# Performance work log

Hardware: AMD Instinct MI355X
Metric: run time of the kernel (lower is better)

Reference implementation:

```python
import jax, jax.numpy as jnp
import numpy as np
from functools import partial

B = 256          # batch_size (== hidden_dim, required by the module's broadcasting)
T = 512          # seq_length
H = 256          # hidden_dim == dim_out
E = 6            # emb_dim
V = 10           # num_input_digits
C = 10           # num_classes


def _kaiming(key, shape):
    fan_in = shape[1]
    return jax.random.normal(key, shape, dtype=jnp.float32) * np.sqrt(2.0 / fan_in)


def setup_inputs() -> dict:
    key = jax.random.key(0)
    ks = jax.random.split(key, 12)
    inp = {
        "x": jax.random.randint(ks[0], (B, T), 0, V),
        "emb": jax.random.normal(ks[1], (V, E), dtype=jnp.float32),
        "Wxg": _kaiming(ks[2], (H, E)), "Whg": _kaiming(ks[3], (H, H)), "bg": jnp.zeros((H,), jnp.float32),
        "Wxi": _kaiming(ks[4], (H, E)), "Whi": _kaiming(ks[5], (H, H)), "bi": jnp.zeros((H,), jnp.float32),
        "Wxf": _kaiming(ks[6], (H, E)), "Whf": _kaiming(ks[7], (H, H)), "bf": jnp.zeros((H,), jnp.float32),
        "Wxo": _kaiming(ks[8], (H, E)), "Who": _kaiming(ks[9], (H, H)), "bo": jnp.zeros((H,), jnp.float32),
        "Wp": _kaiming(ks[10], (C, H)), "bp": jnp.zeros((C,), jnp.float32),
    }
    return inp


def reference(x, emb, Wxg, Whg, bg, Wxi, Whi, bi, Wxf, Whf, bf, Wxo, Who, bo, Wp, bp):
    # x: (B, T) int -> embed -> (B, T, E)
    xe = emb[x]
    # time-major (T, E, B): each step uses x_t.T as in the torch code
    xt_seq = jnp.transpose(xe, (1, 2, 0))

    h0 = jnp.zeros((H, B), jnp.float32)  # h lives as (H, B) per original math
    c0 = jnp.zeros((H, B), jnp.float32)

    def step(carry, xTt):  # xTt: (E, B)
        h, c = carry
        # NOTE: bias (H,) broadcasts over the trailing batch axis (H==B), faithful
        # to the original torch broadcasting.
        g = jnp.tanh(Wxg @ xTt + Whg @ h + bg)
        i = jax.nn.sigmoid(Wxi @ xTt + Whi @ h + bi)
        f = jax.nn.sigmoid(Wxf @ xTt + Whf @ h + bf)
        o = jax.nn.sigmoid(Wxo @ xTt + Who @ h + bo)
        c = g * i + c * f
        h = jnp.tanh(c) * o
        return (h, c), None

    (h, c), _ = jax.lax.scan(step, (h0, c0), xt_seq)
    return (Wp @ h).T + bp  # (B, C)
```

## Files before the change

### kernel.cpp

```cpp
#include <hip/hip_runtime.h>
#include <hip/hip_bf16.h>


typedef __attribute__((ext_vector_type(4))) int   int4v;
typedef __attribute__((ext_vector_type(4))) float float4v;

#define MFMA_I8(a, b, c) __builtin_amdgcn_mfma_i32_16x16x64_i8(a, b, c, 0, 0, 0)

#define K_TANH (-2.8853900817779268f)
#define K_SIG  (-1.4426950408889634f)

__device__ __forceinline__ short f2b(float f) {
    __hip_bfloat16 b = __float2bfloat16(f); return *(short*)&b;
}
__device__ __forceinline__ float b2f(short s) {
    union { unsigned int u; float f; } v; v.u = ((unsigned int)(unsigned short)s) << 16; return v.f;
}
__device__ __forceinline__ float fexp2(float x) {
#if __has_builtin(__builtin_amdgcn_exp2f)
    return __builtin_amdgcn_exp2f(x);
#else
    return __expf(x * 0.6931471805599453f);
#endif
}
__device__ __forceinline__ float frcp(float x) { return __builtin_amdgcn_rcpf(x); }

__global__ __attribute__((amdgpu_flat_work_group_size(512, 512), amdgpu_waves_per_eu(2, 2)))
void lstm_i8(
    const int* __restrict__ x,
    const float* __restrict__ emb,
    const float* __restrict__ Wxg, const float* __restrict__ Whg, const float* __restrict__ bg,
    const float* __restrict__ Wxi, const float* __restrict__ Whi, const float* __restrict__ bi,
    const float* __restrict__ Wxf, const float* __restrict__ Whf, const float* __restrict__ bff,
    const float* __restrict__ Wxo, const float* __restrict__ Who, const float* __restrict__ bo,
    const float* __restrict__ Wp, const float* __restrict__ bp,
    float* __restrict__ out)
{
    const int tid = threadIdx.x, bid = blockIdx.x;
    const int c0 = bid * 2;
    const int w = tid >> 6, lane = tid & 63;
    const int l = lane & 15, q = lane >> 4;
    const int col = l & 1;
    const int g3  = (l >> 1) & 7;
    const int si  = g3 & 3;
    const int srr = g3 >> 2;
    const int rw  = 32 * w;
    const int row = rw + 16 * srr + 4 * q + si;

    __shared__ __align__(16) unsigned int hbuf[2][2 * 272 / 4];
    __shared__ __align__(16) short hfin[2 * 264];
    __shared__ unsigned char xdig2[512 * 2];
    __shared__ __align__(16) float tblf[256 * 44];
    __shared__ float scaleL[4 * 256];

    const float* WxT[4] = {Wxg, Wxi, Wxf, Wxo};
    const float* WhT[4] = {Whg, Whi, Whf, Who};

    if (tid < 2 * 272 / 4) hbuf[0][tid] = 0u;
    for (int i = tid; i < 1024; i += 512)
        xdig2[i] = (unsigned char)x[(c0 + (i & 1)) * 512 + (i >> 1)];

    for (int i = tid; i < 2560; i += 512) {
        int r = i / 10, d = i - r * 10;
        float4v v;
        #pragma unroll
        for (int g = 0; g < 4; g++) {
            float s = 0.f;
            #pragma unroll
            for (int e = 0; e < 6; e++) s += WxT[g][r * 6 + e] * emb[d * 6 + e];
            v[g] = s * (g == 0 ? K_TANH : K_SIG);
        }
        *(float4v*)&tblf[r * 44 + d * 4] = v;
    }

    int4v wa[4][2][4];
    #pragma unroll
    for (int g = 0; g < 4; g++)
        #pragma unroll
        for (int rr = 0; rr < 2; rr++) {
            const float* Wr = WhT[g] + (rw + 16 * rr + l) * 256 + q * 16;
            float mx = 0.f;
            #pragma unroll
            for (int kt = 0; kt < 4; kt++)
                #pragma unroll
                for (int c4 = 0; c4 < 4; c4++) {
                    float4v v = *(const float4v*)(Wr + kt * 64 + c4 * 4);
                    #pragma unroll
                    for (int j = 0; j < 4; j++) mx = fmaxf(mx, fabsf(v[j]));
                }
            mx = fmaxf(mx, __shfl_xor(mx, 16));
            mx = fmaxf(mx, __shfl_xor(mx, 32));
            mx = fmaxf(mx, 1e-20f);
            if (q == 0) scaleL[g * 256 + rw + 16 * rr + l] = mx;
            float qs = 127.f / mx;
            #pragma unroll
            for (int kt = 0; kt < 4; kt++) {
                int4v f;
                #pragma unroll
                for (int dw = 0; dw < 4; dw++) {
                    float4v v = *(const float4v*)(Wr + kt * 64 + dw * 4);
                    int word = 0;
                    #pragma unroll
                    for (int byt = 0; byt < 4; byt++) {
                        int z = (int)rintf(v[byt] * qs);
                        word |= (z & 255) << (8 * byt);
                    }
                    f[dw] = word;
                }
                wa[g][rr][kt] = f;
            }
        }

    __syncthreads();

    float dscl[4];
    #pragma unroll
    for (int g = 0; g < 4; g++) {
        float kk = (g == 0 ? K_TANH : K_SIG) * (1.f / 16129.f);
        dscl[g] = scaleL[g * 256 + row] * kk;
    }
    float bSc[4];
    bSc[0] = bg[c0 + col] * K_TANH; bSc[1] = bi[c0 + col] * K_SIG;
    bSc[2] = bff[c0 + col] * K_SIG; bSc[3] = bo[c0 + col] * K_SIG;

    const bool bi1 = (si & 1) != 0;
    const bool bi2 = (si & 2) != 0;
    const bool brr = (srr != 0);
    const float* tprow = &tblf[row * 44];

    float cs = 0.f, hl = 0.f;

    for (int t = 0; t < 512; t++) {
        const int p = t & 1;
        const char* hbase = (const char*)hbuf[p] + col * 272 + q * 16;

        int4v acc[4][2];
        #pragma unroll
        for (int g = 0; g < 4; g++)
            #pragma unroll
            for (int rr = 0; rr < 2; rr++)
                acc[g][rr] = (int4v){0, 0, 0, 0};

        int dg = xdig2[t * 2 + col];
        float4v tb = *(const float4v*)(tprow + dg * 4);

        #pragma unroll
        for (int kt = 0; kt < 4; kt++) {
            int4v hf = *(const int4v*)(hbase + kt * 64);
            #pragma unroll
            for (int g = 0; g < 4; g++) {
                acc[g][0] = MFMA_I8(wa[g][0][kt], hf, acc[g][0]);
                acc[g][1] = MFMA_I8(wa[g][1][kt], hf, acc[g][1]);
            }
        }

        int av[4];
        #pragma unroll
        for (int g = 0; g < 4; g++) {
            int s00 = bi1 ? acc[g][0][1] : acc[g][0][0];
            int s01 = bi1 ? acc[g][0][3] : acc[g][0][2];
            int s10 = bi1 ? acc[g][1][1] : acc[g][1][0];
            int s11 = bi1 ? acc[g][1][3] : acc[g][1][2];
            int s0  = bi2 ? s01 : s00;
            int s1  = bi2 ? s11 : s10;
            av[g]   = brr ? s1 : s0;
        }
        {
            float pg = fmaf((float)av[0], dscl[0], tb[0] + bSc[0]);
            float pi = fmaf((float)av[1], dscl[1], tb[1] + bSc[1]);
            float pf = fmaf((float)av[2], dscl[2], tb[2] + bSc[2]);
            float po = fmaf((float)av[3], dscl[3], tb[3] + bSc[3]);
            float gg = fmaf(2.f, frcp(1.f + fexp2(pg)), -1.f);
            float ii = frcp(1.f + fexp2(pi));
            float ff = frcp(1.f + fexp2(pf));
            float oo = frcp(1.f + fexp2(po));
            float c  = fmaf(gg, ii, cs * ff);
            cs = c;
            float th = fmaf(2.f, frcp(1.f + fexp2(K_TANH * c)), -1.f);
            float hh = th * oo;
            hl = hh;
            int hq = (int)rintf(hh * 127.f);
            *((char*)hbuf[1 - p] + col * 272 + row) = (char)hq;
        }
        __syncthreads();
    }

    hfin[col * 264 + row] = f2b(hl);
    __syncthreads();

    if (tid < 20) {
        int pc = tid / 10, cls = tid - pc * 10;
        const short* hcol = &hfin[pc * 264];
        const float* wrow = Wp + cls * 256;
        float s = 0.f;
        #pragma unroll 8
        for (int k = 0; k < 256; k++) s += b2f(hcol[k]) * wrow[k];
        out[(c0 + pc) * 10 + cls] = s + bp[cls];
    }
}

extern "C" void kernel_launch(void* const* d_in, const int* in_sizes, int n_in,
                              void* d_out, int out_size, void* d_ws, size_t ws_size,
                              hipStream_t stream) {
    const int*   x   = (const int*)d_in[0];
    const float* emb = (const float*)d_in[1];
    const float* Wxg = (const float*)d_in[2];
    const float* Whg = (const float*)d_in[3];
    const float* bg  = (const float*)d_in[4];
    const float* Wxi = (const float*)d_in[5];
    const float* Whi = (const float*)d_in[6];
    const float* bi  = (const float*)d_in[7];
    const float* Wxf = (const float*)d_in[8];
    const float* Whf = (const float*)d_in[9];
    const float* bff = (const float*)d_in[10];
    const float* Wxo = (const float*)d_in[11];
    const float* Who = (const float*)d_in[12];
    const float* bo  = (const float*)d_in[13];
    const float* Wp  = (const float*)d_in[14];
    const float* bp  = (const float*)d_in[15];

    hipLaunchKernelGGL(lstm_i8, dim3(128), dim3(512), 0, stream,
                       x, emb, Wxg, Whg, bg, Wxi, Whi, bi, Wxf, Whf, bff,
                       Wxo, Who, bo, Wp, bp, (float*)d_out);
}
```

Baseline: 611.0 us.

## Pack h bytes via shuffles, transpose input table, merge reciprocals in gates

Each step now writes the quantized hidden state as one packed 32-bit word per four rows, built from lane shuffles, instead of four separate byte stores. The hbuf stride is changed and the per-digit input table becomes digit-major. The gate math merges reciprocals: tanh(g)*sigmoid(i) and tanh(c)*sigmoid(o) each take a single rcp of a product, with pre-activations clamped so the products cannot overflow. The aim is fewer LDS stores and bank conflicts and fewer transcendental ops on the serial per-step path, at the cost of extra shuffle latency.

```diff
diff --git a/kernel.cpp b/kernel.cpp
--- a/kernel.cpp
+++ b/kernel.cpp
@@ -9,6 +9,8 @@
 
 #define K_TANH (-2.8853900817779268f)
 #define K_SIG  (-1.4426950408889634f)
+
+#define HSTRIDE 320
 
 __device__ __forceinline__ short f2b(float f) {
     __hip_bfloat16 b = __float2bfloat16(f); return *(short*)&b;
@@ -24,6 +26,7 @@
 #endif
 }
 __device__ __forceinline__ float frcp(float x) { return __builtin_amdgcn_rcpf(x); }
+__device__ __forceinline__ float clamp60(float x) { return __builtin_amdgcn_fmed3f(x, -60.f, 60.f); }
 
 __global__ __attribute__((amdgpu_flat_work_group_size(512, 512), amdgpu_waves_per_eu(2, 2)))
 void lstm_i8(
@@ -47,21 +50,21 @@
     const int rw  = 32 * w;
     const int row = rw + 16 * srr + 4 * q + si;
 
-    __shared__ __align__(16) unsigned int hbuf[2][2 * 272 / 4];
+    __shared__ __align__(16) unsigned int hbuf[2][2 * HSTRIDE / 4];
     __shared__ __align__(16) short hfin[2 * 264];
     __shared__ unsigned char xdig2[512 * 2];
-    __shared__ __align__(16) float tblf[256 * 44];
+    __shared__ __align__(16) float tblT[10 * 1024];
     __shared__ float scaleL[4 * 256];
 
     const float* WxT[4] = {Wxg, Wxi, Wxf, Wxo};
     const float* WhT[4] = {Whg, Whi, Whf, Who};
 
-    if (tid < 2 * 272 / 4) hbuf[0][tid] = 0u;
+    if (tid < 2 * HSTRIDE / 4) hbuf[0][tid] = 0u;
     for (int i = tid; i < 1024; i += 512)
         xdig2[i] = (unsigned char)x[(c0 + (i & 1)) * 512 + (i >> 1)];
 
     for (int i = tid; i < 2560; i += 512) {
-        int r = i / 10, d = i - r * 10;
+        int d = i >> 8, r = i & 255;
         float4v v;
         #pragma unroll
         for (int g = 0; g < 4; g++) {
@@ -70,7 +73,7 @@
             for (int e = 0; e < 6; e++) s += WxT[g][r * 6 + e] * emb[d * 6 + e];
             v[g] = s * (g == 0 ? K_TANH : K_SIG);
         }
-        *(float4v*)&tblf[r * 44 + d * 4] = v;
+        *(float4v*)&tblT[d * 1024 + r * 4] = v;
     }
 
     int4v wa[4][2][4];
@@ -126,13 +129,14 @@
     const bool bi1 = (si & 1) != 0;
     const bool bi2 = (si & 2) != 0;
     const bool brr = (srr != 0);
-    const float* tprow = &tblf[row * 44];
+    const float* tprow = tblT + row * 4;
+    const int hoff = col * HSTRIDE + rw + 16 * srr + 4 * q;
 
     float cs = 0.f, hl = 0.f;
 
     for (int t = 0; t < 512; t++) {
         const int p = t & 1;
-        const char* hbase = (const char*)hbuf[p] + col * 272 + q * 16;
+        const char* hbase = (const char*)hbuf[p] + col * HSTRIDE + q * 16;
 
         int4v acc[4][2];
         #pragma unroll
@@ -142,7 +146,7 @@
                 acc[g][rr] = (int4v){0, 0, 0, 0};
 
         int dg = xdig2[t * 2 + col];
-        float4v tb = *(const float4v*)(tprow + dg * 4);
+        float4v tb = *(const float4v*)(tprow + dg * 1024);
 
         #pragma unroll
         for (int kt = 0; kt < 4; kt++) {
@@ -166,21 +170,22 @@
             av[g]   = brr ? s1 : s0;
         }
         {
-            float pg = fmaf((float)av[0], dscl[0], tb[0] + bSc[0]);
-            float pi = fmaf((float)av[1], dscl[1], tb[1] + bSc[1]);
-            float pf = fmaf((float)av[2], dscl[2], tb[2] + bSc[2]);
-            float po = fmaf((float)av[3], dscl[3], tb[3] + bSc[3]);
-            float gg = fmaf(2.f, frcp(1.f + fexp2(pg)), -1.f);
-            float ii = frcp(1.f + fexp2(pi));
-            float ff = frcp(1.f + fexp2(pf));
-            float oo = frcp(1.f + fexp2(po));
-            float c  = fmaf(gg, ii, cs * ff);
+            float pg = clamp60(fmaf((float)av[0], dscl[0], tb[0] + bSc[0]));
+            float pi = clamp60(fmaf((float)av[1], dscl[1], tb[1] + bSc[1]));
+            float pf = clamp60(fmaf((float)av[2], dscl[2], tb[2] + bSc[2]));
+            float po = clamp60(fmaf((float)av[3], dscl[3], tb[3] + bSc[3]));
+            float Eg = fexp2(pg), Ei = fexp2(pi), Ef = fexp2(pf), Eo = fexp2(po);
+            float t1 = (1.f - Eg) * frcp((1.f + Eg) * (1.f + Ei));
+            float c  = fmaf(cs, frcp(1.f + Ef), t1);
             cs = c;
-            float th = fmaf(2.f, frcp(1.f + fexp2(K_TANH * c)), -1.f);
-            float hh = th * oo;
+            float Ec = fexp2(clamp60(K_TANH * c));
+            float hh = (1.f - Ec) * frcp((1.f + Ec) * (1.f + Eo));
             hl = hh;
-            int hq = (int)rintf(hh * 127.f);
-            *((char*)hbuf[1 - p] + col * 272 + row) = (char)hq;
+            int hq = (int)rintf(hh * 127.f) & 255;
+            int w1 = hq | (__shfl_xor(hq, 2) << 8);
+            int w2 = w1 | (__shfl_xor(w1, 4) << 16);
+            if (si == 0)
+                *(int*)((char*)hbuf[1 - p] + hoff) = w2;
         }
         __syncthreads();
     }
```

Result: slower. 635.2 us (+4.0%).
